# Kernel optimization log

Hardware: AMD Instinct MI355X
Metric: run time of the kernel (lower is better)

The kernel has to match this reference:

```python
import jax, jax.numpy as jnp
import numpy as np
import math

N_HEAD = 16
ROPE_BASE = 10000.0


def _rope(xh):
    # xh: [B, H, T, D]; rotate full head dim using half-split (GPT-NeoX style)
    B, H, T, D = xh.shape
    theta = 1.0 / (ROPE_BASE ** (jnp.arange(0, D, 2, dtype=jnp.float32) / D))  # [D/2]
    idx_theta = jnp.arange(T, dtype=jnp.float32)[:, None] * theta[None, :]      # [T, D/2]
    idx_theta2 = jnp.concatenate([idx_theta, idx_theta], axis=1)                 # [T, D]
    cos = jnp.cos(idx_theta2)[None, None]                                        # [1,1,T,D]
    sin = jnp.sin(idx_theta2)[None, None]
    d2 = D // 2
    neg_half = jnp.concatenate([-xh[..., d2:], xh[..., :d2]], axis=-1)
    return xh * cos + neg_half * sin


def setup_inputs() -> dict:
    key = jax.random.key(0)
    k1, k2, k3 = jax.random.split(key, 3)
    B, T, C = 2, 2048, 2048
    x = jax.random.normal(k1, (B, T, C), dtype=jnp.float32)
    w_attn = jax.random.normal(k2, (C, 3 * C), dtype=jnp.float32) * (1.0 / math.sqrt(C))
    w_proj = jax.random.normal(k3, (C, C), dtype=jnp.float32) * (1.0 / math.sqrt(C))
    return {"x": x, "w_attn": w_attn, "w_proj": w_proj}


def reference(x, w_attn, w_proj):
    B, T, C = x.shape
    H = N_HEAD
    D = C // H
    qkv = x @ w_attn                                   # [B,T,3C]
    q, k, v = jnp.split(qkv, 3, axis=-1)
    # [B,T,C] -> [B,H,T,D]
    to_heads = lambda t: t.reshape(B, T, H, D).transpose(0, 2, 1, 3)
    q, k, v = to_heads(q), to_heads(k), to_heads(v)
    q = _rope(q)
    k = _rope(k)
    att = jnp.einsum('bhqd,bhkd->bhqk', q, k) * (1.0 / math.sqrt(D))
    causal = jnp.tril(jnp.ones((T, T), dtype=bool))
    att = jnp.where(causal[None, None], att, -jnp.inf)
    att = jax.nn.softmax(att, axis=-1)
    y = jnp.einsum('bhqk,bhkd->bhqd', att, v)          # [B,H,T,D]
    y = y.transpose(0, 2, 1, 3).reshape(B, T, C)
    return y @ w_proj
```

## Files before the change

kernel.cpp:

```cpp
#include <hip/hip_runtime.h>
#include <hip/hip_bf16.h>
#include <math.h>

typedef __bf16 bf16;
typedef __bf16 bf16x8 __attribute__((ext_vector_type(8)));
typedef float f32x4 __attribute__((ext_vector_type(4)));
typedef float f32x16 __attribute__((ext_vector_type(16)));
typedef unsigned int u32x2 __attribute__((ext_vector_type(2)));
typedef unsigned int u32x4 __attribute__((ext_vector_type(4)));

#define MFMA16(a, b, c) __builtin_amdgcn_mfma_f32_16x16x32_bf16((a), (b), (c), 0, 0, 0)
#define MFMA32(a, b, c) __builtin_amdgcn_mfma_f32_32x32x16_bf16((a), (b), (c), 0, 0, 0)

static constexpr int Bsz = 2, Tsz = 2048, Csz = 2048, Hn = 16, Dh = 128;
static constexpr float ATTN_SCALE = 0.08838834764831845f;

__device__ __forceinline__ void gld16(const void* src, void* dst) {
    __builtin_amdgcn_global_load_lds((__attribute__((address_space(1))) void*)src,
                                     (__attribute__((address_space(3))) void*)dst,
                                     16, 0, 0);
}

__device__ __forceinline__ unsigned cvt_pk_bf16(float lo, float hi) {
    unsigned r;
    asm("v_cvt_pk_bf16_f32 %0, %1, %2" : "=v"(r) : "v"(lo), "v"(hi));
    return r;
}

__device__ __forceinline__ bf16x8 make_pfrag(float p0, float p1, float p2, float p3,
                                             float p4, float p5, float p6, float p7) {
    unsigned a0 = cvt_pk_bf16(p0, p1), a1 = cvt_pk_bf16(p2, p3);
    unsigned b0 = cvt_pk_bf16(p4, p5), b1 = cvt_pk_bf16(p6, p7);
    asm volatile("v_permlane32_swap_b32 %0, %1" : "+v"(a0), "+v"(b0));
    asm volatile("v_permlane32_swap_b32 %0, %1" : "+v"(a1), "+v"(b1));
    u32x4 w = {a0, a1, b0, b1};
    return __builtin_bit_cast(bf16x8, w);
}

__global__ __launch_bounds__(256) void cast_x_kernel(const float* __restrict__ x,
                                                     bf16* __restrict__ o, int n8) {
    int i = blockIdx.x * 256 + threadIdx.x;
    if (i >= n8) return;
    const float4* x4 = (const float4*)x;
    float4 a = x4[2 * i], b = x4[2 * i + 1];
    bf16x8 v;
    v[0] = (bf16)a.x; v[1] = (bf16)a.y; v[2] = (bf16)a.z; v[3] = (bf16)a.w;
    v[4] = (bf16)b.x; v[5] = (bf16)b.y; v[6] = (bf16)b.z; v[7] = (bf16)b.w;
    ((bf16x8*)o)[i] = v;
}

template <typename TIN>
__global__ __launch_bounds__(256) void transpose_cast_kernel(const TIN* __restrict__ in,
                                                             bf16* __restrict__ out,
                                                             int R, int Cc) {
    __shared__ float tile[64][65];
    const int tx = threadIdx.x, ty = threadIdx.y;
    in  += (size_t)blockIdx.z * R * Cc;
    out += (size_t)blockIdx.z * R * Cc;
    const int c0 = blockIdx.x * 64, r0 = blockIdx.y * 64;
#pragma unroll
    for (int j = 0; j < 16; ++j) {
        int rr = ty + j * 4;
        tile[rr][tx] = (float)in[(size_t)(r0 + rr) * Cc + c0 + tx];
    }
    __syncthreads();
#pragma unroll
    for (int j = 0; j < 16; ++j) {
        int cc = ty + j * 4;
        out[(size_t)(c0 + cc) * R + r0 + tx] = (bf16)tile[tx][cc];
    }
}

__global__ __launch_bounds__(256) void cossin_kernel(float2* __restrict__ cs) {
    int idx = blockIdx.x * 256 + threadIdx.x;
    int t = idx >> 6, i = idx & 63;
    float theta = 1.0f / powf(10000.0f, (float)(2 * i) / 128.0f);
    float ang = (float)t * theta;
    cs[idx] = make_float2(cosf(ang), sinf(ang));
}

__global__ __launch_bounds__(512, 2)
void gemm384_qkv(const bf16* __restrict__ A, const bf16* __restrict__ Bt,
                 bf16* __restrict__ Oq, bf16* __restrict__ Ok, bf16* __restrict__ Ov,
                 const float2* __restrict__ cs, int K) {
    __shared__ bf16 sA[2][128 * 64];
    __shared__ bf16 sB[2][384 * 64];
    const int tid = threadIdx.x, lane = tid & 63, wid = tid >> 6;
    const int wm = wid >> 2, wn = wid & 3;
    const int lo16 = lane & 15, hi4 = lane >> 4;

    const int cpx = gridDim.x >> 3;
    const int swz = (blockIdx.x & 7) * cpx + (blockIdx.x >> 3);
    const int by = swz & 31;
    const int bx = swz >> 5;
    const int row0 = by << 7, col0 = bx * 384;

    const int srow = tid >> 3;
    const int swzoff = (((tid & 7) ^ ((tid >> 3) & 7)) << 3);
    const bf16* srcA = A  + (size_t)(row0 + srow) * K + swzoff;
    const bf16* srcB = Bt + (size_t)(col0 + srow) * K + swzoff;
    const size_t K64 = (size_t)K * 64;
    char* const ldsA = (char*)&sA[0][0];
    char* const ldsB = (char*)&sB[0][0];
    const int wuo = wid << 10;

    auto issueA = [&](int c, int kt) {
        const bf16* s = srcA + (size_t)kt * 64;
        gld16(s,       ldsA + c * 16384 + 0    + wuo);
        gld16(s + K64, ldsA + c * 16384 + 8192 + wuo);
    };
    auto issueB = [&](int c, int kt, int u) {
        const bf16* s = srcB + (size_t)kt * 64 + (size_t)(2 * u) * K64;
        gld16(s,       ldsB + c * 49152 + u * 16384 + 0    + wuo);
        gld16(s + K64, ldsB + c * 49152 + u * 16384 + 8192 + wuo);
    };
    auto ldF = [&](const char* buf, int row, int ks) {
        return *(const bf16x8*)(buf + row * 128 + ((((ks << 2) + hi4) ^ (row & 7)) << 4));
    };

    const int arow = (wm << 6) + lo16;
    const int brow = (wn << 4) + lo16;

    f32x4 acc[4][6] = {};
    const int nkt = K >> 6;

    issueA(0, 0); issueB(0, 0, 0); issueB(0, 0, 1); issueB(0, 0, 2);
    asm volatile("s_waitcnt vmcnt(4)" ::: "memory");
    __builtin_amdgcn_s_barrier();

    for (int kt = 0; kt < nkt - 1; ++kt) {
        const int c = kt & 1;
        const char* bufA = ldsA + c * 16384;
        const char* bufB = ldsB + c * 49152;
        bf16x8 af[4][2], bq[2][2];
#pragma unroll
        for (int i = 0; i < 4; ++i) {
            af[i][0] = ldF(bufA, arow + (i << 4), 0);
            af[i][1] = ldF(bufA, arow + (i << 4), 1);
        }
#pragma unroll
        for (int j = 0; j < 2; ++j) {
            bq[j][0] = ldF(bufB, brow + (j << 6), 0);
            bq[j][1] = ldF(bufB, brow + (j << 6), 1);
        }
        issueA(c ^ 1, kt + 1); issueB(c ^ 1, kt + 1, 0); issueB(c ^ 1, kt + 1, 1);
        __builtin_amdgcn_s_barrier();
        asm volatile("s_waitcnt lgkmcnt(0)" ::: "memory");
        __builtin_amdgcn_sched_barrier(0);
        __builtin_amdgcn_s_setprio(1);
#pragma unroll
        for (int ks = 0; ks < 2; ++ks)
#pragma unroll
            for (int i = 0; i < 4; ++i)
#pragma unroll
                for (int j = 0; j < 2; ++j)
                    acc[i][j] = MFMA16(af[i][ks], bq[j][ks], acc[i][j]);
        __builtin_amdgcn_s_setprio(0);
        asm volatile("s_waitcnt vmcnt(8)" ::: "memory");
        __builtin_amdgcn_s_barrier();
#pragma unroll
        for (int j = 0; j < 2; ++j) {
            bq[j][0] = ldF(bufB, brow + ((j + 2) << 6), 0);
            bq[j][1] = ldF(bufB, brow + ((j + 2) << 6), 1);
        }
        issueB(c ^ 1, kt + 1, 2);
        __builtin_amdgcn_s_barrier();
        asm volatile("s_waitcnt lgkmcnt(0)" ::: "memory");
        __builtin_amdgcn_sched_barrier(0);
        __builtin_amdgcn_s_setprio(1);
#pragma unroll
        for (int ks = 0; ks < 2; ++ks)
#pragma unroll
            for (int i = 0; i < 4; ++i)
#pragma unroll
                for (int j = 0; j < 2; ++j)
                    acc[i][j + 2] = MFMA16(af[i][ks], bq[j][ks], acc[i][j + 2]);
        __builtin_amdgcn_s_setprio(0);
        asm volatile("s_waitcnt vmcnt(8)" ::: "memory");
        __builtin_amdgcn_s_barrier();
#pragma unroll
        for (int j = 0; j < 2; ++j) {
            bq[j][0] = ldF(bufB, brow + ((j + 4) << 6), 0);
            bq[j][1] = ldF(bufB, brow + ((j + 4) << 6), 1);
        }
        __builtin_amdgcn_s_barrier();
        asm volatile("s_waitcnt lgkmcnt(0)" ::: "memory");
        __builtin_amdgcn_sched_barrier(0);
        __builtin_amdgcn_s_setprio(1);
#pragma unroll
        for (int ks = 0; ks < 2; ++ks)
#pragma unroll
            for (int i = 0; i < 4; ++i)
#pragma unroll
                for (int j = 0; j < 2; ++j)
                    acc[i][j + 4] = MFMA16(af[i][ks], bq[j][ks], acc[i][j + 4]);
        __builtin_amdgcn_s_setprio(0);
        asm volatile("s_waitcnt vmcnt(4)" ::: "memory");
        __builtin_amdgcn_s_barrier();
    }

    {
        const int c = (nkt - 1) & 1;
        const char* bufA = ldsA + c * 16384;
        const char* bufB = ldsB + c * 49152;
        bf16x8 af[4][2], bq[2][2];
#pragma unroll
        for (int i = 0; i < 4; ++i) {
            af[i][0] = ldF(bufA, arow + (i << 4), 0);
            af[i][1] = ldF(bufA, arow + (i << 4), 1);
        }
#pragma unroll
        for (int j = 0; j < 2; ++j) {
            bq[j][0] = ldF(bufB, brow + (j << 6), 0);
            bq[j][1] = ldF(bufB, brow + (j << 6), 1);
        }
        __builtin_amdgcn_s_barrier();
        asm volatile("s_waitcnt lgkmcnt(0)" ::: "memory");
        __builtin_amdgcn_sched_barrier(0);
        __builtin_amdgcn_s_setprio(1);
#pragma unroll
        for (int ks = 0; ks < 2; ++ks)
#pragma unroll
            for (int i = 0; i < 4; ++i)
#pragma unroll
                for (int j = 0; j < 2; ++j)
                    acc[i][j] = MFMA16(af[i][ks], bq[j][ks], acc[i][j]);
        __builtin_amdgcn_s_setprio(0);
        asm volatile("s_waitcnt vmcnt(2)" ::: "memory");
        __builtin_amdgcn_s_barrier();
#pragma unroll
        for (int j = 0; j < 2; ++j) {
            bq[j][0] = ldF(bufB, brow + ((j + 2) << 6), 0);
            bq[j][1] = ldF(bufB, brow + ((j + 2) << 6), 1);
        }
        __builtin_amdgcn_s_barrier();
        asm volatile("s_waitcnt lgkmcnt(0)" ::: "memory");
        __builtin_amdgcn_sched_barrier(0);
        __builtin_amdgcn_s_setprio(1);
#pragma unroll
        for (int ks = 0; ks < 2; ++ks)
#pragma unroll
            for (int i = 0; i < 4; ++i)
#pragma unroll
                for (int j = 0; j < 2; ++j)
                    acc[i][j + 2] = MFMA16(af[i][ks], bq[j][ks], acc[i][j + 2]);
        __builtin_amdgcn_s_setprio(0);
        asm volatile("s_waitcnt vmcnt(0)" ::: "memory");
        __builtin_amdgcn_s_barrier();
#pragma unroll
        for (int j = 0; j < 2; ++j) {
            bq[j][0] = ldF(bufB, brow + ((j + 4) << 6), 0);
            bq[j][1] = ldF(bufB, brow + ((j + 4) << 6), 1);
        }
        __builtin_amdgcn_s_barrier();
        asm volatile("s_waitcnt lgkmcnt(0)" ::: "memory");
        __builtin_amdgcn_sched_barrier(0);
        __builtin_amdgcn_s_setprio(1);
#pragma unroll
        for (int ks = 0; ks < 2; ++ks)
#pragma unroll
            for (int i = 0; i < 4; ++i)
#pragma unroll
                for (int j = 0; j < 2; ++j)
                    acc[i][j + 4] = MFMA16(af[i][ks], bq[j][ks], acc[i][j + 4]);
        __builtin_amdgcn_s_setprio(0);
    }

    const int d = (wn << 4) + lo16;
#pragma unroll
    for (int p = 0; p < 3; ++p) {
        const int gcb = col0 + (p << 7);
        const int seg = gcb >> 11;
        const int hb = (gcb >> 7) & 15;
        if (seg < 2) {
            bf16* dst0 = (seg == 0) ? Oq : Ok;
            const float qs = (seg == 0) ? ATTN_SCALE : 1.0f;
#pragma unroll
            for (int mi = 0; mi < 4; ++mi)
#pragma unroll
                for (int r = 0; r < 4; ++r) {
                    const int gm = row0 + (wm << 6) + (mi << 4) + (hi4 << 2) + r;
                    const int b = gm >> 11, t = gm & 2047;
                    const float2 csv = cs[t * 64 + d];
                    bf16* drow = dst0 + ((((size_t)b * Hn + hb) * Tsz + t) << 7);
                    const float vlo = acc[mi][2 * p][r];
                    const float vhi = acc[mi][2 * p + 1][r];
                    drow[d]      = (bf16)((vlo * csv.x - vhi * csv.y) * qs);
                    drow[d + 64] = (bf16)((vhi * csv.x + vlo * csv.y) * qs);
                }
        } else {
#pragma unroll
            for (int mi = 0; mi < 4; ++mi)
#pragma unroll
                for (int r = 0; r < 4; ++r) {
                    const int gm = row0 + (wm << 6) + (mi << 4) + (hi4 << 2) + r;
                    const int b = gm >> 11, t = gm & 2047;
                    bf16* drow = Ov + ((((size_t)b * Hn + hb) * Tsz + t) << 7);
                    drow[d]      = (bf16)acc[mi][2 * p][r];
                    drow[d + 64] = (bf16)acc[mi][2 * p + 1][r];
                }
        }
    }
}

__global__ __launch_bounds__(512, 2)
void gemm256_proj(const bf16* __restrict__ A, const bf16* __restrict__ Bt,
                  float* __restrict__ Cf, int K) {
    __shared__ bf16 sA[2][128 * 64];
    __shared__ bf16 sB[2][256 * 64];
    const int tid = threadIdx.x, lane = tid & 63, wid = tid >> 6;
    const int wm = wid >> 2, wn = wid & 3;
    const int lo16 = lane & 15, hi4 = lane >> 4;
    const int N = 2048;

    const int cpx = gridDim.x >> 3;
    const int swz = (blockIdx.x & 7) * cpx + (blockIdx.x >> 3);
    const int by = swz & 31;
    const int bx = swz >> 5;
    const int row0 = by << 7, col0 = bx << 8;

    const int srow = tid >> 3;
    const int swzoff = (((tid & 7) ^ ((tid >> 3) & 7)) << 3);
    const bf16* srcA = A  + (size_t)(row0 + srow) * K + swzoff;
    const bf16* srcB = Bt + (size_t)(col0 + srow) * K + swzoff;
    const size_t K64 = (size_t)K * 64;
    char* const ldsA = (char*)&sA[0][0];
    char* const ldsB = (char*)&sB[0][0];
    const int wuo = wid << 10;

    auto issueA = [&](int c, int kt) {
        const bf16* s = srcA + (size_t)kt * 64;
        gld16(s,       ldsA + c * 16384 + 0    + wuo);
        gld16(s + K64, ldsA + c * 16384 + 8192 + wuo);
    };
    auto issueB = [&](int c, int kt, int u) {
        const bf16* s = srcB + (size_t)kt * 64 + (size_t)(2 * u) * K64;
        gld16(s,       ldsB + c * 32768 + u * 16384 + 0    + wuo);
        gld16(s + K64, ldsB + c * 32768 + u * 16384 + 8192 + wuo);
    };
    auto ldF = [&](const char* buf, int row, int ks) {
        return *(const bf16x8*)(buf + row * 128 + ((((ks << 2) + hi4) ^ (row & 7)) << 4));
    };

    const int arow = (wm << 6) + lo16;
    const int brow = (wn << 4) + lo16;

    f32x4 acc[4][4] = {};
    const int nkt = K >> 6;

    issueA(0, 0); issueB(0, 0, 0); issueB(0, 0, 1);
    if (nkt > 1) { issueA(1, 1); issueB(1, 1, 0); }
    asm volatile("s_waitcnt vmcnt(4)" ::: "memory");
    __builtin_amdgcn_s_barrier();

    for (int kt = 0; kt < nkt; ++kt) {
        const int c = kt & 1;
        const char* bufA = ldsA + c * 16384;
        const char* bufB = ldsB + c * 32768;
        bf16x8 af[4][2], bq[2][2];
#pragma unroll
        for (int i = 0; i < 4; ++i) {
            af[i][0] = ldF(bufA, arow + (i << 4), 0);
            af[i][1] = ldF(bufA, arow + (i << 4), 1);
        }
#pragma unroll
        for (int j = 0; j < 2; ++j) {
            bq[j][0] = ldF(bufB, brow + (j << 6), 0);
            bq[j][1] = ldF(bufB, brow + (j << 6), 1);
        }
        if (kt + 1 < nkt) issueB(c ^ 1, kt + 1, 1);
        __builtin_amdgcn_s_barrier();
        asm volatile("s_waitcnt lgkmcnt(0)" ::: "memory");
        __builtin_amdgcn_sched_barrier(0);
        __builtin_amdgcn_s_setprio(1);
#pragma unroll
        for (int ks = 0; ks < 2; ++ks)
#pragma unroll
            for (int i = 0; i < 4; ++i)
#pragma unroll
                for (int j = 0; j < 2; ++j)
                    acc[i][j] = MFMA16(af[i][ks], bq[j][ks], acc[i][j]);
        __builtin_amdgcn_s_setprio(0);
        if (kt + 1 < nkt) asm volatile("s_waitcnt vmcnt(6)" ::: "memory");
        else              asm volatile("s_waitcnt vmcnt(0)" ::: "memory");
        __builtin_amdgcn_s_barrier();
#pragma unroll
        for (int j = 0; j < 2; ++j) {
            bq[j][0] = ldF(bufB, brow + ((j + 2) << 6), 0);
            bq[j][1] = ldF(bufB, brow + ((j + 2) << 6), 1);
        }
        if (kt + 2 < nkt) { issueA(c, kt + 2); issueB(c, kt + 2, 0); }
        __builtin_amdgcn_s_barrier();
        asm volatile("s_waitcnt lgkmcnt(0)" ::: "memory");
        __builtin_amdgcn_sched_barrier(0);
        __builtin_amdgcn_s_setprio(1);
#pragma unroll
        for (int ks = 0; ks < 2; ++ks)
#pragma unroll
            for (int i = 0; i < 4; ++i)
#pragma unroll
                for (int j = 0; j < 2; ++j)
                    acc[i][j + 2] = MFMA16(af[i][ks], bq[j][ks], acc[i][j + 2]);
        __builtin_amdgcn_s_setprio(0);
        if (kt + 2 < nkt)      asm volatile("s_waitcnt vmcnt(6)" ::: "memory");
        else if (kt + 1 < nkt) asm volatile("s_waitcnt vmcnt(2)" ::: "memory");
        __builtin_amdgcn_s_barrier();
    }

#pragma unroll
    for (int mi = 0; mi < 4; ++mi)
#pragma unroll
        for (int r = 0; r < 4; ++r) {
            const int gm = row0 + (wm << 6) + (mi << 4) + (hi4 << 2) + r;
            float* crow = Cf + (size_t)gm * N + col0 + (wn << 4) + lo16;
#pragma unroll
            for (int nj = 0; nj < 4; ++nj)
                crow[nj << 6] = acc[mi][nj][r];
        }
}

__device__ __forceinline__ void stage_tile(const bf16* __restrict__ Kb,
                                           const bf16* __restrict__ Vtb,
                                           bf16* sKc, bf16* sVc, int k0, int tid) {
#pragma unroll
    for (int c = 0; c < 4; ++c) {
        const int off = (c << 12) + (tid << 4);
        const int row = off >> 8, u = (off >> 4) & 15;
        gld16(Kb + (size_t)(k0 + row) * Dh + ((u ^ (row & 7)) << 3), (char*)sKc + off);
        const int dv = off >> 7, uv = (off >> 4) & 7;
        gld16(Vtb + (size_t)dv * Tsz + k0 + ((uv ^ (dv & 7)) << 3), (char*)sVc + off);
    }
}

__global__ __launch_bounds__(256, 2)
void attn_kernel(const bf16* __restrict__ Q, const bf16* __restrict__ K,
                 const bf16* __restrict__ Vt, bf16* __restrict__ Y) {
    __shared__ bf16 sK[2][64 * 128];
    __shared__ bf16 sV[2][128 * 64];
    const int tid = threadIdx.x, lane = tid & 63, wv = tid >> 6;
    const int lo32 = lane & 31, hl = lane >> 5;

    const int i = blockIdx.x;
    const int g = i >> 5;
    const int bh = i & 31;
    const int t = (i < 256) ? (15 - g) : (g - 8);
    const int b = bh >> 4, h = bh & 15;

    const int q0 = t << 7;
    const int q0w = q0 + (wv << 5);
    const int qg = q0w + lo32;

    const bf16* Kb  = K  + (size_t)bh * (Tsz * Dh);
    const bf16* Vtb = Vt + (size_t)bh * (Tsz * Dh);
    const bf16* Qp  = Q  + (size_t)bh * (Tsz * Dh) + (size_t)qg * Dh;

    bf16x8 qf[8];
#pragma unroll
    for (int kc = 0; kc < 8; ++kc)
        qf[kc] = *(const bf16x8*)(Qp + (kc << 4) + (hl << 3));

    float m = -1e30f, lsum = 0.f;
    f32x16 o[4] = {};

    const int nt_block = 2 * t + 2;
    const int nt_warp = ((q0w + 31) >> 6) + 1;

    stage_tile(Kb, Vtb, &sK[0][0], &sV[0][0], 0, tid);

    int cur = 0;
    for (int kt = 0; kt < nt_block; ++kt) {
        __syncthreads();
        if (kt + 1 < nt_block)
            stage_tile(Kb, Vtb, &sK[cur ^ 1][0], &sV[cur ^ 1][0], (kt + 1) << 6, tid);
        if (kt < nt_warp) {
            const int k0 = kt << 6;
            const bf16* kbuf = &sK[cur][0];
            const bf16* vbuf = &sV[cur][0];
            f32x16 s0 = {}, s1 = {};
            const int swk = lo32 & 7;
            __builtin_amdgcn_s_setprio(1);
#pragma unroll
            for (int kc = 0; kc < 8; ++kc) {
                bf16x8 kf0 = *(const bf16x8*)((const char*)kbuf + lo32 * 256 +
                              ((((kc << 1) + hl) ^ swk) << 4));
                s0 = MFMA32(kf0, qf[kc], s0);
                bf16x8 kf1 = *(const bf16x8*)((const char*)kbuf + (32 + lo32) * 256 +
                              ((((kc << 1) + hl) ^ swk) << 4));
                s1 = MFMA32(kf1, qf[kc], s1);
            }
            __builtin_amdgcn_s_setprio(0);

            const bool bnd = (k0 + 63 > q0w);
            if (bnd) {
#pragma unroll
                for (int r = 0; r < 16; ++r) {
                    const int kl = (r & 3) + ((r >> 2) << 3) + (hl << 2);
                    if (k0 + kl > qg)      s0[r] = -1e30f;
                    if (k0 + 32 + kl > qg) s1[r] = -1e30f;
                }
            }
            float pm = s0[0];
#pragma unroll
            for (int r = 1; r < 16; ++r) pm = fmaxf(pm, s0[r]);
#pragma unroll
            for (int r = 0; r < 16; ++r) pm = fmaxf(pm, s1[r]);
            pm = fmaxf(pm, __shfl_xor(pm, 32));

            if (__any(pm > m + 8.0f)) {
                const float mn = fmaxf(m, pm);
                const float sc = __expf(m - mn);
                m = mn;
                lsum *= sc;
#pragma unroll
                for (int db = 0; db < 4; ++db)
#pragma unroll
                    for (int r = 0; r < 16; ++r) o[db][r] *= sc;
            }
            float rs = 0.f;
            if (bnd) {
#pragma unroll
                for (int r = 0; r < 16; ++r) {
                    float e0 = (s0[r] > -1e29f) ? __expf(s0[r] - m) : 0.f;
                    float e1 = (s1[r] > -1e29f) ? __expf(s1[r] - m) : 0.f;
                    s0[r] = e0; s1[r] = e1; rs += e0 + e1;
                }
            } else {
#pragma unroll
                for (int r = 0; r < 16; ++r) {
                    float e0 = __expf(s0[r] - m);
                    float e1 = __expf(s1[r] - m);
                    s0[r] = e0; s1[r] = e1; rs += e0 + e1;
                }
            }
            rs += __shfl_xor(rs, 32);
            lsum += rs;

            bf16x8 pb0 = make_pfrag(s0[0], s0[1], s0[2],  s0[3],  s0[4],  s0[5],  s0[6],  s0[7]);
            bf16x8 pb1 = make_pfrag(s0[8], s0[9], s0[10], s0[11], s0[12], s0[13], s0[14], s0[15]);
            bf16x8 pb2 = make_pfrag(s1[0], s1[1], s1[2],  s1[3],  s1[4],  s1[5],  s1[6],  s1[7]);
            bf16x8 pb3 = make_pfrag(s1[8], s1[9], s1[10], s1[11], s1[12], s1[13], s1[14], s1[15]);

            __builtin_amdgcn_s_setprio(1);
#pragma unroll
            for (int db = 0; db < 4; ++db) {
                const int rd = (db << 5) + lo32;
                const char* vrow = (const char*)vbuf + rd * 128;
                const int sw = rd & 7;
                bf16x8 v0 = *(const bf16x8*)(vrow + (((0 + hl) ^ sw) << 4));
                o[db] = MFMA32(v0, pb0, o[db]);
                bf16x8 v1 = *(const bf16x8*)(vrow + (((2 + hl) ^ sw) << 4));
                o[db] = MFMA32(v1, pb1, o[db]);
                bf16x8 v2 = *(const bf16x8*)(vrow + (((4 + hl) ^ sw) << 4));
                o[db] = MFMA32(v2, pb2, o[db]);
                bf16x8 v3 = *(const bf16x8*)(vrow + (((6 + hl) ^ sw) << 4));
                o[db] = MFMA32(v3, pb3, o[db]);
            }
            __builtin_amdgcn_s_setprio(0);
        }
        cur ^= 1;
    }

    const float inv = 1.0f / lsum;
    const size_t rowoff = ((size_t)b * Tsz + qg) * (size_t)Csz + (size_t)h * 128;
#pragma unroll
    for (int db = 0; db < 4; ++db)
#pragma unroll
        for (int gg = 0; gg < 4; ++gg) {
            unsigned w0 = cvt_pk_bf16(o[db][4 * gg + 0] * inv, o[db][4 * gg + 1] * inv);
            unsigned w1 = cvt_pk_bf16(o[db][4 * gg + 2] * inv, o[db][4 * gg + 3] * inv);
            u32x2 w = {w0, w1};
            *(u32x2*)(Y + rowoff + (db << 5) + (gg << 3) + (hl << 2)) = w;
        }
}

extern "C" void kernel_launch(void* const* d_in, const int* in_sizes, int n_in,
                              void* d_out, int out_size, void* d_ws, size_t ws_size,
                              hipStream_t stream) {
    const float* x      = (const float*)d_in[0];
    const float* w_attn = (const float*)d_in[1];
    const float* w_proj = (const float*)d_in[2];
    float* out = (float*)d_out;

    char* ws = (char*)d_ws;
    bf16* Xb  = (bf16*)(ws);
    bf16* Wat = (bf16*)(ws + 16777216);
    bf16* Wpt = (bf16*)(ws + 41943040);
    bf16* Qr  = (bf16*)(ws + 50331648);
    bf16* Kr  = (bf16*)(ws + 67108864);
    bf16* Vb  = (bf16*)(ws + 83886080);
    bf16* Vt  = (bf16*)(ws + 100663296);
    bf16* Yb  = (bf16*)(ws + 117440512);
    float2* cs = (float2*)(ws + 134217728);

    cast_x_kernel<<<4096, 256, 0, stream>>>(x, Xb, (Bsz * Tsz * Csz) / 8);
    transpose_cast_kernel<float><<<dim3(96, 32, 1), dim3(64, 4), 0, stream>>>(w_attn, Wat, 2048, 6144);
    transpose_cast_kernel<float><<<dim3(32, 32, 1), dim3(64, 4), 0, stream>>>(w_proj, Wpt, 2048, 2048);
    cossin_kernel<<<512, 256, 0, stream>>>(cs);

    gemm384_qkv<<<512, 512, 0, stream>>>(Xb, Wat, Qr, Kr, Vb, cs, 2048);
    transpose_cast_kernel<bf16><<<dim3(2, 32, 32), dim3(64, 4), 0, stream>>>(Vb, Vt, 2048, 128);

    attn_kernel<<<dim3(512), 256, 0, stream>>>(Qr, Kr, Vt, Yb);

    gemm256_proj<<<256, 512, 0, stream>>>(Yb, Wpt, out, 2048);
}
```

Before: 239.6 us.

## Replace fine-grained split pipelines in GEMM kernels with simple double-buffered loop

Both the QKV and projection GEMM main loops drop their hand-tuned multi-phase schedules. Those schedules split the B tile into chunks, used partial vmcnt waits, and interleaved barriers. The new loop issues the full next tile's global-to-LDS loads at the top of each iteration, reads all A/B fragments, runs all MFMAs, then calls __syncthreads. This simplifies the code and cuts barriers per iteration, but relies on __syncthreads to drain outstanding vmcnt, which likely exposes global load latency and raises register pressure from holding all B fragments at once.

```diff
diff --git a/kernel.cpp b/kernel.cpp
--- a/kernel.cpp
+++ b/kernel.cpp
@@ -125,145 +125,39 @@
     const int nkt = K >> 6;
 
     issueA(0, 0); issueB(0, 0, 0); issueB(0, 0, 1); issueB(0, 0, 2);
-    asm volatile("s_waitcnt vmcnt(4)" ::: "memory");
-    __builtin_amdgcn_s_barrier();
-
-    for (int kt = 0; kt < nkt - 1; ++kt) {
+    __syncthreads();
+
+    for (int kt = 0; kt < nkt; ++kt) {
         const int c = kt & 1;
         const char* bufA = ldsA + c * 16384;
         const char* bufB = ldsB + c * 49152;
-        bf16x8 af[4][2], bq[2][2];
+        if (kt + 1 < nkt) {
+            issueA(c ^ 1, kt + 1);
+            issueB(c ^ 1, kt + 1, 0);
+            issueB(c ^ 1, kt + 1, 1);
+            issueB(c ^ 1, kt + 1, 2);
+        }
+        bf16x8 af[4][2], bq[6][2];
 #pragma unroll
         for (int i = 0; i < 4; ++i) {
             af[i][0] = ldF(bufA, arow + (i << 4), 0);
             af[i][1] = ldF(bufA, arow + (i << 4), 1);
         }
 #pragma unroll
-        for (int j = 0; j < 2; ++j) {
+        for (int j = 0; j < 6; ++j) {
             bq[j][0] = ldF(bufB, brow + (j << 6), 0);
             bq[j][1] = ldF(bufB, brow + (j << 6), 1);
         }
-        issueA(c ^ 1, kt + 1); issueB(c ^ 1, kt + 1, 0); issueB(c ^ 1, kt + 1, 1);
-        __builtin_amdgcn_s_barrier();
-        asm volatile("s_waitcnt lgkmcnt(0)" ::: "memory");
-        __builtin_amdgcn_sched_barrier(0);
         __builtin_amdgcn_s_setprio(1);
 #pragma unroll
         for (int ks = 0; ks < 2; ++ks)
 #pragma unroll
             for (int i = 0; i < 4; ++i)
 #pragma unroll
-                for (int j = 0; j < 2; ++j)
+                for (int j = 0; j < 6; ++j)
                     acc[i][j] = MFMA16(af[i][ks], bq[j][ks], acc[i][j]);
         __builtin_amdgcn_s_setprio(0);
-        asm volatile("s_waitcnt vmcnt(8)" ::: "memory");
-        __builtin_amdgcn_s_barrier();
-#pragma unroll
-        for (int j = 0; j < 2; ++j) {
-            bq[j][0] = ldF(bufB, brow + ((j + 2) << 6), 0);
-            bq[j][1] = ldF(bufB, brow + ((j + 2) << 6), 1);
-        }
-        issueB(c ^ 1, kt + 1, 2);
-        __builtin_amdgcn_s_barrier();
-        asm volatile("s_waitcnt lgkmcnt(0)" ::: "memory");
-        __builtin_amdgcn_sched_barrier(0);
-        __builtin_amdgcn_s_setprio(1);
-#pragma unroll
-        for (int ks = 0; ks < 2; ++ks)
-#pragma unroll
-            for (int i = 0; i < 4; ++i)
-#pragma unroll
-                for (int j = 0; j < 2; ++j)
-                    acc[i][j + 2] = MFMA16(af[i][ks], bq[j][ks], acc[i][j + 2]);
-        __builtin_amdgcn_s_setprio(0);
-        asm volatile("s_waitcnt vmcnt(8)" ::: "memory");
-        __builtin_amdgcn_s_barrier();
-#pragma unroll
-        for (int j = 0; j < 2; ++j) {
-            bq[j][0] = ldF(bufB, brow + ((j + 4) << 6), 0);
-            bq[j][1] = ldF(bufB, brow + ((j + 4) << 6), 1);
-        }
-        __builtin_amdgcn_s_barrier();
-        asm volatile("s_waitcnt lgkmcnt(0)" ::: "memory");
-        __builtin_amdgcn_sched_barrier(0);
-        __builtin_amdgcn_s_setprio(1);
-#pragma unroll
-        for (int ks = 0; ks < 2; ++ks)
-#pragma unroll
-            for (int i = 0; i < 4; ++i)
-#pragma unroll
-                for (int j = 0; j < 2; ++j)
-                    acc[i][j + 4] = MFMA16(af[i][ks], bq[j][ks], acc[i][j + 4]);
-        __builtin_amdgcn_s_setprio(0);
-        asm volatile("s_waitcnt vmcnt(4)" ::: "memory");
-        __builtin_amdgcn_s_barrier();
-    }
-
-    {
-        const int c = (nkt - 1) & 1;
-        const char* bufA = ldsA + c * 16384;
-        const char* bufB = ldsB + c * 49152;
-        bf16x8 af[4][2], bq[2][2];
-#pragma unroll
-        for (int i = 0; i < 4; ++i) {
-            af[i][0] = ldF(bufA, arow + (i << 4), 0);
-            af[i][1] = ldF(bufA, arow + (i << 4), 1);
-        }
-#pragma unroll
-        for (int j = 0; j < 2; ++j) {
-            bq[j][0] = ldF(bufB, brow + (j << 6), 0);
-            bq[j][1] = ldF(bufB, brow + (j << 6), 1);
-        }
-        __builtin_amdgcn_s_barrier();
-        asm volatile("s_waitcnt lgkmcnt(0)" ::: "memory");
-        __builtin_amdgcn_sched_barrier(0);
-        __builtin_amdgcn_s_setprio(1);
-#pragma unroll
-        for (int ks = 0; ks < 2; ++ks)
-#pragma unroll
-            for (int i = 0; i < 4; ++i)
-#pragma unroll
-                for (int j = 0; j < 2; ++j)
-                    acc[i][j] = MFMA16(af[i][ks], bq[j][ks], acc[i][j]);
-        __builtin_amdgcn_s_setprio(0);
-        asm volatile("s_waitcnt vmcnt(2)" ::: "memory");
-        __builtin_amdgcn_s_barrier();
-#pragma unroll
-        for (int j = 0; j < 2; ++j) {
-            bq[j][0] = ldF(bufB, brow + ((j + 2) << 6), 0);
-            bq[j][1] = ldF(bufB, brow + ((j + 2) << 6), 1);
-        }
-        __builtin_amdgcn_s_barrier();
-        asm volatile("s_waitcnt lgkmcnt(0)" ::: "memory");
-        __builtin_amdgcn_sched_barrier(0);
-        __builtin_amdgcn_s_setprio(1);
-#pragma unroll
-        for (int ks = 0; ks < 2; ++ks)
-#pragma unroll
-            for (int i = 0; i < 4; ++i)
-#pragma unroll
-                for (int j = 0; j < 2; ++j)
-                    acc[i][j + 2] = MFMA16(af[i][ks], bq[j][ks], acc[i][j + 2]);
-        __builtin_amdgcn_s_setprio(0);
-        asm volatile("s_waitcnt vmcnt(0)" ::: "memory");
-        __builtin_amdgcn_s_barrier();
-#pragma unroll
-        for (int j = 0; j < 2; ++j) {
-            bq[j][0] = ldF(bufB, brow + ((j + 4) << 6), 0);
-            bq[j][1] = ldF(bufB, brow + ((j + 4) << 6), 1);
-        }
-        __builtin_amdgcn_s_barrier();
-        asm volatile("s_waitcnt lgkmcnt(0)" ::: "memory");
-        __builtin_amdgcn_sched_barrier(0);
-        __builtin_amdgcn_s_setprio(1);
-#pragma unroll
-        for (int ks = 0; ks < 2; ++ks)
-#pragma unroll
-            for (int i = 0; i < 4; ++i)
-#pragma unroll
-                for (int j = 0; j < 2; ++j)
-                    acc[i][j + 4] = MFMA16(af[i][ks], bq[j][ks], acc[i][j + 4]);
-        __builtin_amdgcn_s_setprio(0);
+        __syncthreads();
     }
 
     const int d = (wn << 4) + lo16;
@@ -349,62 +243,38 @@
     const int nkt = K >> 6;
 
     issueA(0, 0); issueB(0, 0, 0); issueB(0, 0, 1);
-    if (nkt > 1) { issueA(1, 1); issueB(1, 1, 0); }
-    asm volatile("s_waitcnt vmcnt(4)" ::: "memory");
-    __builtin_amdgcn_s_barrier();
+    __syncthreads();
 
     for (int kt = 0; kt < nkt; ++kt) {
         const int c = kt & 1;
         const char* bufA = ldsA + c * 16384;
         const char* bufB = ldsB + c * 32768;
-        bf16x8 af[4][2], bq[2][2];
+        if (kt + 1 < nkt) {
+            issueA(c ^ 1, kt + 1);
+            issueB(c ^ 1, kt + 1, 0);
+            issueB(c ^ 1, kt + 1, 1);
+        }
+        bf16x8 af[4][2], bq[4][2];
 #pragma unroll
         for (int i = 0; i < 4; ++i) {
             af[i][0] = ldF(bufA, arow + (i << 4), 0);
             af[i][1] = ldF(bufA, arow + (i << 4), 1);
         }
 #pragma unroll
-        for (int j = 0; j < 2; ++j) {
+        for (int j = 0; j < 4; ++j) {
             bq[j][0] = ldF(bufB, brow + (j << 6), 0);
             bq[j][1] = ldF(bufB, brow + (j << 6), 1);
         }
-        if (kt + 1 < nkt) issueB(c ^ 1, kt + 1, 1);
-        __builtin_amdgcn_s_barrier();
-        asm volatile("s_waitcnt lgkmcnt(0)" ::: "memory");
-        __builtin_amdgcn_sched_barrier(0);
         __builtin_amdgcn_s_setprio(1);
 #pragma unroll
         for (int ks = 0; ks < 2; ++ks)
 #pragma unroll
             for (int i = 0; i < 4; ++i)
 #pragma unroll
-                for (int j = 0; j < 2; ++j)
+                for (int j = 0; j < 4; ++j)
                     acc[i][j] = MFMA16(af[i][ks], bq[j][ks], acc[i][j]);
         __builtin_amdgcn_s_setprio(0);
-        if (kt + 1 < nkt) asm volatile("s_waitcnt vmcnt(6)" ::: "memory");
-        else              asm volatile("s_waitcnt vmcnt(0)" ::: "memory");
-        __builtin_amdgcn_s_barrier();
-#pragma unroll
-        for (int j = 0; j < 2; ++j) {
-            bq[j][0] = ldF(bufB, brow + ((j + 2) << 6), 0);
-            bq[j][1] = ldF(bufB, brow + ((j + 2) << 6), 1);
-        }
-        if (kt + 2 < nkt) { issueA(c, kt + 2); issueB(c, kt + 2, 0); }
-        __builtin_amdgcn_s_barrier();
-        asm volatile("s_waitcnt lgkmcnt(0)" ::: "memory");
-        __builtin_amdgcn_sched_barrier(0);
-        __builtin_amdgcn_s_setprio(1);
-#pragma unroll
-        for (int ks = 0; ks < 2; ++ks)
-#pragma unroll
-            for (int i = 0; i < 4; ++i)
-#pragma unroll
-                for (int j = 0; j < 2; ++j)
-                    acc[i][j + 2] = MFMA16(af[i][ks], bq[j][ks], acc[i][j + 2]);
-        __builtin_amdgcn_s_setprio(0);
-        if (kt + 2 < nkt)      asm volatile("s_waitcnt vmcnt(6)" ::: "memory");
-        else if (kt + 1 < nkt) asm volatile("s_waitcnt vmcnt(2)" ::: "memory");
-        __builtin_amdgcn_s_barrier();
+        __syncthreads();
     }
 
 #pragma unroll
```

New measurement: 275.8 us. +15.1%, slower.

## Write V transposed directly from QKV GEMM epilogue and vectorize transpose stores

Applied to the files above, without the earlier changes.

The QKV GEMM epilogue now writes V straight into the transposed [B,H,D,T] layout, packing four consecutive time steps into 8-byte stores. This removes the separate V transpose kernel along with its extra global round trip. The weight transpose-cast kernel also switches its stores to 4-wide bf16 vectors instead of scalar stores. In exchange, the epilogue writes V with a large stride across d, which may coalesce less well than the old row-major write.

```diff
diff --git a/kernel.cpp b/kernel.cpp
--- a/kernel.cpp
+++ b/kernel.cpp
@@ -4,6 +4,7 @@
 
 typedef __bf16 bf16;
 typedef __bf16 bf16x8 __attribute__((ext_vector_type(8)));
+typedef __bf16 bf16x4v __attribute__((ext_vector_type(4)));
 typedef float f32x4 __attribute__((ext_vector_type(4)));
 typedef float f32x16 __attribute__((ext_vector_type(16)));
 typedef unsigned int u32x2 __attribute__((ext_vector_type(2)));
@@ -64,10 +65,17 @@
         tile[rr][tx] = (float)in[(size_t)(r0 + rr) * Cc + c0 + tx];
     }
     __syncthreads();
-#pragma unroll
-    for (int j = 0; j < 16; ++j) {
-        int cc = ty + j * 4;
-        out[(size_t)(c0 + cc) * R + r0 + tx] = (bf16)tile[tx][cc];
+    const int q = (tx & 15) << 2;
+    const int cg = tx >> 4;
+#pragma unroll
+    for (int j = 0; j < 4; ++j) {
+        const int cc = j * 16 + cg * 4 + ty;
+        bf16x4v v;
+        v[0] = (bf16)tile[q + 0][cc];
+        v[1] = (bf16)tile[q + 1][cc];
+        v[2] = (bf16)tile[q + 2][cc];
+        v[3] = (bf16)tile[q + 3][cc];
+        *(bf16x4v*)(out + (size_t)(c0 + cc) * R + r0 + q) = v;
     }
 }
 
@@ -81,7 +89,7 @@
 
 __global__ __launch_bounds__(512, 2)
 void gemm384_qkv(const bf16* __restrict__ A, const bf16* __restrict__ Bt,
-                 bf16* __restrict__ Oq, bf16* __restrict__ Ok, bf16* __restrict__ Ov,
+                 bf16* __restrict__ Oq, bf16* __restrict__ Ok, bf16* __restrict__ Vt,
                  const float2* __restrict__ cs, int K) {
     __shared__ bf16 sA[2][128 * 64];
     __shared__ bf16 sB[2][384 * 64];
@@ -290,15 +298,17 @@
                 }
         } else {
 #pragma unroll
-            for (int mi = 0; mi < 4; ++mi)
-#pragma unroll
-                for (int r = 0; r < 4; ++r) {
-                    const int gm = row0 + (wm << 6) + (mi << 4) + (hi4 << 2) + r;
-                    const int b = gm >> 11, t = gm & 2047;
-                    bf16* drow = Ov + ((((size_t)b * Hn + hb) * Tsz + t) << 7);
-                    drow[d]      = (bf16)acc[mi][2 * p][r];
-                    drow[d + 64] = (bf16)acc[mi][2 * p + 1][r];
-                }
+            for (int mi = 0; mi < 4; ++mi) {
+                const int t0 = row0 + (wm << 6) + (mi << 4) + (hi4 << 2);
+                const int b = t0 >> 11, tt = t0 & 2047;
+                bf16* vbase = Vt + (((size_t)b * Hn + hb) * Dh) * Tsz + tt;
+                u32x2 wlo = {cvt_pk_bf16(acc[mi][2 * p][0], acc[mi][2 * p][1]),
+                             cvt_pk_bf16(acc[mi][2 * p][2], acc[mi][2 * p][3])};
+                u32x2 whi = {cvt_pk_bf16(acc[mi][2 * p + 1][0], acc[mi][2 * p + 1][1]),
+                             cvt_pk_bf16(acc[mi][2 * p + 1][2], acc[mi][2 * p + 1][3])};
+                *(u32x2*)(vbase + (size_t)d * Tsz)        = wlo;
+                *(u32x2*)(vbase + (size_t)(d + 64) * Tsz) = whi;
+            }
         }
     }
 }
@@ -587,7 +597,6 @@
     bf16* Wpt = (bf16*)(ws + 41943040);
     bf16* Qr  = (bf16*)(ws + 50331648);
     bf16* Kr  = (bf16*)(ws + 67108864);
-    bf16* Vb  = (bf16*)(ws + 83886080);
     bf16* Vt  = (bf16*)(ws + 100663296);
     bf16* Yb  = (bf16*)(ws + 117440512);
     float2* cs = (float2*)(ws + 134217728);
@@ -597,8 +606,7 @@
     transpose_cast_kernel<float><<<dim3(32, 32, 1), dim3(64, 4), 0, stream>>>(w_proj, Wpt, 2048, 2048);
     cossin_kernel<<<512, 256, 0, stream>>>(cs);
 
-    gemm384_qkv<<<512, 512, 0, stream>>>(Xb, Wat, Qr, Kr, Vb, cs, 2048);
-    transpose_cast_kernel<bf16><<<dim3(2, 32, 32), dim3(64, 4), 0, stream>>>(Vb, Vt, 2048, 128);
+    gemm384_qkv<<<512, 512, 0, stream>>>(Xb, Wat, Qr, Kr, Vt, cs, 2048);
 
     attn_kernel<<<dim3(512), 256, 0, stream>>>(Qr, Kr, Vt, Yb);
 
```

Result: no change. 235.0 us (-1.9%).
